# Kernel tuning notes

Measured on AMD Instinct MI355X. Metric: run time of the kernel, lower is better.

## Reference

```python
import jax, jax.numpy as jnp
import numpy as np

IMG = 640
TOPK = 13
NC = 1
ALPHA = 0.5
BETA = 6.0
EPS = 1e-9
IOU_EPS = 1e-7


def _make_anchors():
    pts = []
    for s in (8, 16, 32):
        n = IMG // s
        g = (jnp.arange(n, dtype=jnp.float32) + 0.5) * s
        yy, xx = jnp.meshgrid(g, g, indexing="ij")
        pts.append(jnp.stack([xx.ravel(), yy.ravel()], axis=-1))
    return jnp.concatenate(pts, axis=0)  # [8400, 2]


def _make_boxes(key, prefix):
    k1, k2 = jax.random.split(key)
    cxcy = jax.random.uniform(k1, prefix + (2,), minval=32.0, maxval=IMG - 32.0)
    wh = jax.random.uniform(k2, prefix + (2,), minval=8.0, maxval=128.0)
    return jnp.concatenate([cxcy - wh / 2, cxcy + wh / 2], axis=-1)


def setup_inputs() -> dict:
    key = jax.random.key(0)
    B, G, NA = 32, 64, 8400
    k1, k2, k3, k4 = jax.random.split(key, 4)
    pd_scores = jax.random.uniform(k1, (B, NA, 1))
    pd_bboxes = _make_boxes(k2, (B, NA))
    anc_points = _make_anchors()
    gt_labels = jnp.zeros((B, G, 1), dtype=jnp.int64)  # single class
    gt_bboxes = _make_boxes(k3, (B, G))
    num_gt = jax.random.randint(k4, (B, 1), 1, G + 1)
    mask_gt = (jnp.arange(G)[None, :] < num_gt).astype(jnp.float32)[..., None]
    return {
        "pd_scores": pd_scores,
        "pd_bboxes": pd_bboxes,
        "anc_points": anc_points,
        "gt_labels": gt_labels,
        "gt_bboxes": gt_bboxes,
        "mask_gt": mask_gt,
    }


def _iou_xyxy(gt, pd):
    # gt: [B,G,1,4], pd: [B,1,NA,4] -> [B,G,NA]
    ix1 = jnp.maximum(gt[..., 0], pd[..., 0])
    iy1 = jnp.maximum(gt[..., 1], pd[..., 1])
    ix2 = jnp.minimum(gt[..., 2], pd[..., 2])
    iy2 = jnp.minimum(gt[..., 3], pd[..., 3])
    inter = jnp.clip(ix2 - ix1, 0) * jnp.clip(iy2 - iy1, 0)
    a1 = (gt[..., 2] - gt[..., 0]) * (gt[..., 3] - gt[..., 1])
    a2 = (pd[..., 2] - pd[..., 0]) * (pd[..., 3] - pd[..., 1])
    return inter / (a1 + a2 - inter + IOU_EPS)


def reference(pd_scores, pd_bboxes, anc_points, gt_labels, gt_bboxes, mask_gt):
    B, G, _ = gt_bboxes.shape
    NA = pd_bboxes.shape[1]

    # candidates inside GT boxes: [B,G,NA]
    ap = anc_points[None, None]                   # [1,1,NA,2]
    gb = gt_bboxes[:, :, None]                    # [B,G,1,4]
    lt = ap - gb[..., :2]
    rb = gb[..., 2:] - ap
    mask_in_gts = (jnp.concatenate([lt, rb], axis=-1).min(axis=-1) > 0).astype(jnp.float32)
    valid_mask = mask_in_gts * mask_gt[..., 0][:, :, None]

    # pairwise IoU + alignment metric
    overlaps = jnp.clip(_iou_xyxy(gt_bboxes[:, :, None], pd_bboxes[:, None]), 0)  # [B,G,NA]
    bbox_scores = pd_scores[..., 0][:, None, :]                                   # [B,1,NA]
    align_metric = jnp.clip(bbox_scores, 0) ** ALPHA * overlaps ** BETA * valid_mask

    # top-k per GT over anchors (threshold-based mask, including ties, like torch ref)
    k = min(TOPK, NA)
    topk_vals = jax.lax.top_k(align_metric, k)[0]          # [B,G,k]
    threshold = topk_vals[..., -1:]
    mask_topk = (align_metric >= threshold).astype(jnp.float32)

    mask_pos = mask_topk * valid_mask

    # conflict resolution: anchor claimed by >1 GT -> GT with max IoU
    fg = mask_pos.sum(axis=1)                              # [B,NA]
    disputed = fg[:, None, :] > 1                          # [B,1,NA]
    best_gt = jnp.argmax(overlaps, axis=1)                 # [B,NA]
    one_hot_gt = (jnp.arange(G)[None, :, None] == best_gt[:, None, :]).astype(jnp.float32)
    mask_pos = jnp.where(disputed, one_hot_gt, mask_pos)
    fg_mask = mask_pos.sum(axis=1)                         # [B,NA]
    target_gt_idx = jnp.argmax(mask_pos, axis=1)           # [B,NA]

    # gather targets
    target_labels = jnp.clip(
        jnp.take_along_axis(gt_labels[..., 0], target_gt_idx, axis=1), 0)      # [B,NA]
    target_bboxes = jnp.take_along_axis(gt_bboxes, target_gt_idx[..., None], axis=1)  # [B,NA,4]
    target_scores = jax.nn.one_hot(target_labels, NC, dtype=jnp.float32) * fg_mask[..., None]

    # alignment normalization
    am = align_metric * mask_pos
    pos_align_max = am.max(axis=-1, keepdims=True)
    pos_iou_max = (overlaps * mask_pos).max(axis=-1, keepdims=True)
    norm_weights = (am / (pos_align_max + EPS) * pos_iou_max).max(axis=1)       # [B,NA]
    target_scores = target_scores * norm_weights[..., None]

    return target_labels, target_bboxes, target_scores, fg_mask > 0
```

## Files before the change

### kernel.cpp

```cpp
#include <hip/hip_runtime.h>

#define TOPK_K 13
#define KPAD 16
#define PCAP 384


__device__ __forceinline__ float iou_clip(const float4 g, const float4 p) {
    float ix1 = fmaxf(g.x, p.x), iy1 = fmaxf(g.y, p.y);
    float ix2 = fminf(g.z, p.z), iy2 = fminf(g.w, p.w);
    float iw = fmaxf(ix2 - ix1, 0.f);
    float ih = fmaxf(iy2 - iy1, 0.f);
    float inter = iw * ih;
    float a1 = (g.z - g.x) * (g.w - g.y);
    float a2 = (p.z - p.x) * (p.w - p.y);
    float iou = inter / (a1 + a2 - inter + 1e-7f);
    return fmaxf(iou, 0.f);
}

__device__ __forceinline__ float in_box(float ax, float ay, const float4 g) {
    float m = fminf(fminf(ax - g.x, ay - g.y), fminf(g.z - ax, g.w - ay));
    return (m > 0.f) ? 1.f : 0.f;
}

__device__ __forceinline__ float align_metric_f(float sqs, float iou, float valid) {
    float p2 = iou * iou;
    float p6 = p2 * p2 * p2;
    return sqs * p6 * valid;
}

__device__ __forceinline__ void anc_xy(int i, float& ax, float& ay) {
    int lvl = (i < 6400) ? 0 : (i < 8000 ? 1 : 2);
    int n   = (lvl == 0) ? 80 : (lvl == 1 ? 40 : 20);
    int off = (lvl == 0) ? 0  : (lvl == 1 ? 6400 : 8000);
    float sf = (float)(8 << lvl);
    int r = i - off;
    int iy = r / n, ix = r - iy * n;
    ax = (ix + 0.5f) * sf;
    ay = (iy + 0.5f) * sf;
}

__global__ __launch_bounds__(256) void k_thresh(
    const float* __restrict__ pd_scores, const float* __restrict__ pd_bboxes,
    const float* __restrict__ gt_bboxes, const float* __restrict__ mask_gt,
    float* __restrict__ thr, int* __restrict__ pam, int* __restrict__ pim,
    int B, int G, int NA)
{
    __shared__ float plist[PCAP];
    __shared__ int   pcnt;

    int w = blockIdx.x;
    int tid = threadIdx.x;
    if (tid == 0) { pam[w] = 0; pim[w] = 0; pcnt = 0; }
    __syncthreads();

    if (mask_gt[w] == 0.f) { if (tid == 0) thr[w] = 0.f; return; }

    int b = w / G;
    float4 gb = *(const float4*)(gt_bboxes + (size_t)w * 4);
    const float* ps = pd_scores + (size_t)b * NA;
    const float* pb = pd_bboxes + (size_t)b * NA * 4;

    #pragma unroll
    for (int lvl = 0; lvl < 3; ++lvl) {
        const int n   = (lvl == 0) ? 80 : (lvl == 1 ? 40 : 20);
        const int off = (lvl == 0) ? 0  : (lvl == 1 ? 6400 : 8000);
        const float sf = (float)(8 << lvl);
        int ix0 = max(0,     (int)floorf(gb.x / sf - 0.5f));
        int iy0 = max(0,     (int)floorf(gb.y / sf - 0.5f));
        int ix1 = min(n - 1, (int)ceilf (gb.z / sf - 0.5f));
        int iy1 = min(n - 1, (int)ceilf (gb.w / sf - 0.5f));
        int wdt = ix1 - ix0 + 1, hgt = iy1 - iy0 + 1;
        if (wdt <= 0 || hgt <= 0) continue;
        int n_c = wdt * hgt;
        for (int c = tid; c < n_c; c += 256) {
            int ix = ix0 + (c % wdt);
            int iy = iy0 + (c / wdt);
            float ax = (ix + 0.5f) * sf;
            float ay = (iy + 0.5f) * sf;
            if (in_box(ax, ay, gb) != 0.f) {
                int a = off + iy * n + ix;
                float4 p = *(const float4*)(pb + (size_t)a * 4);
                float iou = iou_clip(gb, p);
                float sqs = sqrtf(fmaxf(ps[a], 0.f));
                float am = align_metric_f(sqs, iou, 1.f);
                if (am > 0.f) {
                    int idx = atomicAdd(&pcnt, 1);
                    if (idx < PCAP) plist[idx] = am;
                }
            }
        }
    }
    __syncthreads();

    int n = pcnt;
    if (n < TOPK_K) { if (tid == 0) thr[w] = 0.f; return; }

    if (tid < 64) {
        int lane = tid;
        float t[KPAD];
        #pragma unroll
        for (int i = 0; i < KPAD; ++i) t[i] = 0.f;
        for (int j = lane; j < n; j += 64) {
            float v = plist[j];
            if (v > t[KPAD - 1]) {
                t[KPAD - 1] = v;
                #pragma unroll
                for (int i = KPAD - 1; i > 0; --i) {
                    float hi = fmaxf(t[i - 1], t[i]);
                    float lo = fminf(t[i - 1], t[i]);
                    t[i - 1] = hi; t[i] = lo;
                }
            }
        }
        for (int off = 1; off < 64; off <<= 1) {
            float o[KPAD], m[KPAD];
            #pragma unroll
            for (int i = 0; i < KPAD; ++i) o[i] = __shfl_xor(t[i], off, 64);
            #pragma unroll
            for (int i = 0; i < KPAD; ++i) m[i] = fmaxf(t[i], o[KPAD - 1 - i]);
            #pragma unroll
            for (int s = 8; s >= 1; s >>= 1) {
                #pragma unroll
                for (int i = 0; i < KPAD; ++i) {
                    if ((i & s) == 0) {
                        float hi = fmaxf(m[i], m[i + s]);
                        float lo = fminf(m[i], m[i + s]);
                        m[i] = hi; m[i + s] = lo;
                    }
                }
            }
            #pragma unroll
            for (int i = 0; i < KPAD; ++i) t[i] = m[i];
        }
        if (lane == 0) thr[w] = t[TOPK_K - 1];
    }
}

__global__ __launch_bounds__(256) void k_assign(
    const float* __restrict__ pd_scores, const float* __restrict__ pd_bboxes,
    const int* __restrict__ gt_labels,
    const float* __restrict__ gt_bboxes, const float* __restrict__ mask_gt,
    const float* __restrict__ thr,
    float* __restrict__ out_labels, float* __restrict__ out_bboxes,
    float* __restrict__ out_fg,
    int* __restrict__ ws_tgt, float* __restrict__ ws_amv,
    int* __restrict__ pam, int* __restrict__ pim,
    int B, int G, int NA)
{
    __shared__ float4 sbox[64];
    __shared__ float  smask[64];
    __shared__ float  sthr[64];
    __shared__ int    slab[64];
    __shared__ float  sred[4][4];
    __shared__ int    slist[64];
    __shared__ int    scount;
    __shared__ float4 dbox[256];
    __shared__ int    dtgt[256];
    __shared__ int    dcnt;

    int b = blockIdx.y;
    int tid = threadIdx.x;
    if (tid == 0) dcnt = 0;
    if (tid < 64) {
        sbox[tid]  = *(const float4*)(gt_bboxes + ((size_t)b * G + tid) * 4);
        smask[tid] = mask_gt[b * G + tid];
        sthr[tid]  = thr[b * G + tid];
        int l = gt_labels[b * G + tid];
        slab[tid]  = (l < 0) ? 0 : l;
    }

    int a = blockIdx.x * blockDim.x + tid;
    bool act = (a < NA);
    int lane = tid & 63;
    int wv = tid >> 6;
    int ac = act ? a : (NA - 1);
    size_t o = (size_t)b * NA + ac;

    float ax, ay; anc_xy(ac, ax, ay);

    float mnx = ax, mxx = ax, mny = ay, mxy = ay;
    #pragma unroll
    for (int off = 32; off >= 1; off >>= 1) {
        mnx = fminf(mnx, __shfl_xor(mnx, off, 64));
        mxx = fmaxf(mxx, __shfl_xor(mxx, off, 64));
        mny = fminf(mny, __shfl_xor(mny, off, 64));
        mxy = fmaxf(mxy, __shfl_xor(mxy, off, 64));
    }
    if (lane == 0) { sred[wv][0] = mnx; sred[wv][1] = mxx; sred[wv][2] = mny; sred[wv][3] = mxy; }
    __syncthreads();
    float bmnx = fminf(fminf(sred[0][0], sred[1][0]), fminf(sred[2][0], sred[3][0]));
    float bmxx = fmaxf(fmaxf(sred[0][1], sred[1][1]), fmaxf(sred[2][1], sred[3][1]));
    float bmny = fminf(fminf(sred[0][2], sred[1][2]), fminf(sred[2][2], sred[3][2]));
    float bmxy = fmaxf(fmaxf(sred[0][3], sred[1][3]), fmaxf(sred[2][3], sred[3][3]));

    if (tid < 64) {
        float4 gbb = sbox[tid];
        bool el = (smask[tid] != 0.f) &&
                  (gbb.x < bmxx) && (gbb.z > bmnx) &&
                  (gbb.y < bmxy) && (gbb.w > bmny);
        unsigned long long bal = __ballot(el);
        if (el) slist[(int)__popcll(bal & ((1ull << tid) - 1ull))] = tid;
        if (tid == 0) scount = (int)__popcll(bal);
    }
    __syncthreads();
    int nsl = scount;

    float4 p = *(const float4*)(pd_bboxes + o * 4);
    float sqs = sqrtf(fmaxf(pd_scores[o], 0.f));

    int fg = 0, firstg = 0;
    for (int j = 0; j < nsl; ++j) {
        int g = slist[j];
        float4 gbb = sbox[g];
        if (act && in_box(ax, ay, gbb) != 0.f) {
            float iou = iou_clip(gbb, p);
            float am = align_metric_f(sqs, iou, 1.f);
            if (am >= sthr[g]) { if (fg == 0) firstg = g; ++fg; }
        }
    }

    int tgt = (fg == 1) ? firstg : 0;

    bool disp = (fg > 1);
    int slot = -1;
    if (disp) { slot = atomicAdd(&dcnt, 1); dbox[slot] = p; }
    __syncthreads();
    int nd = dcnt;
    if (tid < nd) {
        float4 pp = dbox[tid];
        float bi = -1.f; int bg = 0;
        #pragma unroll 4
        for (int g = 0; g < 64; ++g) {
            float iou = iou_clip(sbox[g], pp);
            if (iou > bi) { bi = iou; bg = g; }
        }
        dtgt[tid] = bg;
    }
    __syncthreads();
    if (disp) tgt = dtgt[slot];

    if (!act) return;

    float4 gbt = sbox[tgt];
    float vt  = in_box(ax, ay, gbt) * smask[tgt];
    float iout = iou_clip(gbt, p);
    float amt = align_metric_f(sqs, iout, vt);
    bool isfg = (fg != 0);
    float amv = isfg ? amt : 0.f;
    float iov = isfg ? iout : 0.f;

    out_labels[o] = (float)slab[tgt];
    *(float4*)(out_bboxes + o * 4) = gbt;
    out_fg[o] = isfg ? 1.f : 0.f;
    ws_tgt[o] = tgt;
    ws_amv[o] = amv;

    if (isfg) {
        int gi = b * G + tgt;
        atomicMax(&pam[gi], __float_as_int(amv));
        atomicMax(&pim[gi], __float_as_int(iov));
    }
}

__global__ __launch_bounds__(256) void k_scores(
    const int* __restrict__ ws_tgt, const float* __restrict__ ws_amv,
    const int* __restrict__ pam, const int* __restrict__ pim,
    const float* __restrict__ out_labels,
    float* __restrict__ out_scores,
    int B, int G, int NA)
{
    __shared__ int spam[64];
    __shared__ int spim[64];

    int b = blockIdx.y;
    int tid = threadIdx.x;
    if (tid < 64) {
        spam[tid] = pam[b * G + tid];
        spim[tid] = pim[b * G + tid];
    }
    __syncthreads();

    int a = blockIdx.x * blockDim.x + tid;
    if (a >= NA) return;
    size_t o = (size_t)b * NA + a;

    int tgt = ws_tgt[o];
    float amv = ws_amv[o];
    float pa = __int_as_float(spam[tgt]);
    float pi = __int_as_float(spim[tgt]);
    float wgt = amv / (pa + 1e-9f) * pi;
    float onehot = (out_labels[o] == 0.f) ? 1.f : 0.f;
    out_scores[o] = onehot * wgt;
}

extern "C" void kernel_launch(void* const* d_in, const int* in_sizes, int n_in,
                              void* d_out, int out_size, void* d_ws, size_t ws_size,
                              hipStream_t stream) {
    const float* pd_scores = (const float*)d_in[0];
    const float* pd_bboxes = (const float*)d_in[1];
    const int*   gt_labels = (const int*)d_in[3];
    const float* gt_bboxes = (const float*)d_in[4];
    const float* mask_gt   = (const float*)d_in[5];

    int NA = in_sizes[2] / 2;
    int B  = in_sizes[0] / NA;
    int G  = in_sizes[4] / (B * 4);

    float* out = (float*)d_out;
    float* out_labels = out;
    float* out_bboxes = out_labels + (size_t)B * NA;
    float* out_scores = out_bboxes + (size_t)B * NA * 4;
    float* out_fg     = out_scores + (size_t)B * NA;

    int BG = B * G;
    size_t BNA = (size_t)B * NA;
    float* thr    = (float*)d_ws;
    int*   pam    = (int*)(thr + BG);
    int*   pim    = pam + BG;
    int*   ws_tgt = pim + BG;
    float* ws_amv = (float*)(ws_tgt + BNA);

    k_thresh<<<dim3(BG), dim3(256), 0, stream>>>(
        pd_scores, pd_bboxes, gt_bboxes, mask_gt, thr, pam, pim, B, G, NA);

    k_assign<<<dim3((NA + 255) / 256, B), dim3(256), 0, stream>>>(
        pd_scores, pd_bboxes, gt_labels, gt_bboxes, mask_gt, thr,
        out_labels, out_bboxes, out_fg, ws_tgt, ws_amv, pam, pim, B, G, NA);

    k_scores<<<dim3((NA + 255) / 256, B), dim3(256), 0, stream>>>(
        ws_tgt, ws_amv, pam, pim, out_labels, out_scores, B, G, NA);
}
```

Before: 39.54 us.

## Replace global per-GT atomic max with block-local shared atomics and partial reduction

Result: no change. 40.18 us (+1.6%).

```diff
diff --git a/kernel.cpp b/kernel.cpp
--- a/kernel.cpp
+++ b/kernel.cpp
@@ -42,7 +42,7 @@
 __global__ __launch_bounds__(256) void k_thresh(
     const float* __restrict__ pd_scores, const float* __restrict__ pd_bboxes,
     const float* __restrict__ gt_bboxes, const float* __restrict__ mask_gt,
-    float* __restrict__ thr, int* __restrict__ pam, int* __restrict__ pim,
+    float* __restrict__ thr,
     int B, int G, int NA)
 {
     __shared__ float plist[PCAP];
@@ -50,7 +50,7 @@
 
     int w = blockIdx.x;
     int tid = threadIdx.x;
-    if (tid == 0) { pam[w] = 0; pim[w] = 0; pcnt = 0; }
+    if (tid == 0) pcnt = 0;
     __syncthreads();
 
     if (mask_gt[w] == 0.f) { if (tid == 0) thr[w] = 0.f; return; }
@@ -144,13 +144,15 @@
     float* __restrict__ out_labels, float* __restrict__ out_bboxes,
     float* __restrict__ out_fg,
     int* __restrict__ ws_tgt, float* __restrict__ ws_amv,
-    int* __restrict__ pam, int* __restrict__ pim,
-    int B, int G, int NA)
+    int* __restrict__ pam_part, int* __restrict__ pim_part,
+    int B, int G, int NA, int NBX)
 {
     __shared__ float4 sbox[64];
     __shared__ float  smask[64];
     __shared__ float  sthr[64];
     __shared__ int    slab[64];
+    __shared__ int    spam[64];
+    __shared__ int    spim[64];
     __shared__ float  sred[4][4];
     __shared__ int    slist[64];
     __shared__ int    scount;
@@ -167,6 +169,8 @@
         sthr[tid]  = thr[b * G + tid];
         int l = gt_labels[b * G + tid];
         slab[tid]  = (l < 0) ? 0 : l;
+        spam[tid]  = 0;
+        spim[tid]  = 0;
     }
 
     int a = blockIdx.x * blockDim.x + tid;
@@ -239,35 +243,41 @@
     __syncthreads();
     if (disp) tgt = dtgt[slot];
 
-    if (!act) return;
-
-    float4 gbt = sbox[tgt];
-    float vt  = in_box(ax, ay, gbt) * smask[tgt];
-    float iout = iou_clip(gbt, p);
-    float amt = align_metric_f(sqs, iout, vt);
-    bool isfg = (fg != 0);
-    float amv = isfg ? amt : 0.f;
-    float iov = isfg ? iout : 0.f;
-
-    out_labels[o] = (float)slab[tgt];
-    *(float4*)(out_bboxes + o * 4) = gbt;
-    out_fg[o] = isfg ? 1.f : 0.f;
-    ws_tgt[o] = tgt;
-    ws_amv[o] = amv;
-
-    if (isfg) {
-        int gi = b * G + tgt;
-        atomicMax(&pam[gi], __float_as_int(amv));
-        atomicMax(&pim[gi], __float_as_int(iov));
+    if (act) {
+        float4 gbt = sbox[tgt];
+        float vt  = in_box(ax, ay, gbt) * smask[tgt];
+        float iout = iou_clip(gbt, p);
+        float amt = align_metric_f(sqs, iout, vt);
+        bool isfg = (fg != 0);
+        float amv = isfg ? amt : 0.f;
+        float iov = isfg ? iout : 0.f;
+
+        out_labels[o] = (float)slab[tgt];
+        *(float4*)(out_bboxes + o * 4) = gbt;
+        out_fg[o] = isfg ? 1.f : 0.f;
+        ws_tgt[o] = tgt;
+        ws_amv[o] = amv;
+
+        if (isfg) {
+            atomicMax(&spam[tgt], __float_as_int(amv));
+            atomicMax(&spim[tgt], __float_as_int(iov));
+        }
+    }
+    __syncthreads();
+
+    if (tid < 64) {
+        size_t pb_off = ((size_t)b * NBX + blockIdx.x) * 64 + tid;
+        pam_part[pb_off] = spam[tid];
+        pim_part[pb_off] = spim[tid];
     }
 }
 
 __global__ __launch_bounds__(256) void k_scores(
     const int* __restrict__ ws_tgt, const float* __restrict__ ws_amv,
-    const int* __restrict__ pam, const int* __restrict__ pim,
+    const int* __restrict__ pam_part, const int* __restrict__ pim_part,
     const float* __restrict__ out_labels,
     float* __restrict__ out_scores,
-    int B, int G, int NA)
+    int B, int G, int NA, int NBX)
 {
     __shared__ int spam[64];
     __shared__ int spim[64];
@@ -275,8 +285,14 @@
     int b = blockIdx.y;
     int tid = threadIdx.x;
     if (tid < 64) {
-        spam[tid] = pam[b * G + tid];
-        spim[tid] = pim[b * G + tid];
+        int mpa = 0, mpi = 0;
+        for (int j = 0; j < NBX; ++j) {
+            size_t off = ((size_t)b * NBX + j) * 64 + tid;
+            mpa = max(mpa, pam_part[off]);
+            mpi = max(mpi, pim_part[off]);
+        }
+        spam[tid] = mpa;
+        spim[tid] = mpi;
     }
     __syncthreads();
 
@@ -305,6 +321,7 @@
     int NA = in_sizes[2] / 2;
     int B  = in_sizes[0] / NA;
     int G  = in_sizes[4] / (B * 4);
+    int NBX = (NA + 255) / 256;
 
     float* out = (float*)d_out;
     float* out_labels = out;
@@ -314,19 +331,21 @@
 
     int BG = B * G;
     size_t BNA = (size_t)B * NA;
-    float* thr    = (float*)d_ws;
-    int*   pam    = (int*)(thr + BG);
-    int*   pim    = pam + BG;
-    int*   ws_tgt = pim + BG;
-    float* ws_amv = (float*)(ws_tgt + BNA);
+    float* thr      = (float*)d_ws;
+    int*   ws_tgt   = (int*)(thr + BG);
+    float* ws_amv   = (float*)(ws_tgt + BNA);
+    int*   pam_part = (int*)(ws_amv + BNA);
+    int*   pim_part = pam_part + (size_t)B * NBX * 64;
 
     k_thresh<<<dim3(BG), dim3(256), 0, stream>>>(
-        pd_scores, pd_bboxes, gt_bboxes, mask_gt, thr, pam, pim, B, G, NA);
-
-    k_assign<<<dim3((NA + 255) / 256, B), dim3(256), 0, stream>>>(
+        pd_scores, pd_bboxes, gt_bboxes, mask_gt, thr, B, G, NA);
+
+    k_assign<<<dim3(NBX, B), dim3(256), 0, stream>>>(
         pd_scores, pd_bboxes, gt_labels, gt_bboxes, mask_gt, thr,
-        out_labels, out_bboxes, out_fg, ws_tgt, ws_amv, pam, pim, B, G, NA);
-
-    k_scores<<<dim3((NA + 255) / 256, B), dim3(256), 0, stream>>>(
-        ws_tgt, ws_amv, pam, pim, out_labels, out_scores, B, G, NA);
-}
+        out_labels, out_bboxes, out_fg, ws_tgt, ws_amv,
+        pam_part, pim_part, B, G, NA, NBX);
+
+    k_scores<<<dim3(NBX, B), dim3(256), 0, stream>>>(
+        ws_tgt, ws_amv, pam_part, pim_part, out_labels, out_scores,
+        B, G, NA, NBX);
+}
```
